# Kernel optimization log

Hardware: AMD Instinct MI355X
Metric: run time of the kernel (lower is better)

The kernel has to match this reference:

```python
import jax, jax.numpy as jnp
import numpy as np

EMB = 512
HEADS = 8

def setup_inputs() -> dict:
    key = jax.random.key(0)
    ks = jax.random.split(key, 9)
    s = 1.0 / np.sqrt(EMB)
    x = jax.random.normal(ks[0], (32, 4096, EMB), dtype=jnp.float32)
    Wq = jax.random.normal(ks[1], (EMB, EMB), dtype=jnp.float32) * s
    bq = jax.random.normal(ks[2], (EMB,), dtype=jnp.float32) * s
    Wk = jax.random.normal(ks[3], (EMB, EMB), dtype=jnp.float32) * s
    bk = jax.random.normal(ks[4], (EMB,), dtype=jnp.float32) * s
    Wv = jax.random.normal(ks[5], (EMB, EMB), dtype=jnp.float32) * s
    bv = jax.random.normal(ks[6], (EMB,), dtype=jnp.float32) * s
    Wo = jax.random.normal(ks[7], (EMB, EMB), dtype=jnp.float32) * s
    bo = jax.random.normal(ks[8], (EMB,), dtype=jnp.float32) * s
    return {"x": x, "Wq": Wq, "bq": bq, "Wk": Wk, "bk": bk,
            "Wv": Wv, "bv": bv, "Wo": Wo, "bo": bo}

def reference(x, Wq, bq, Wk, bk, Wv, bv, Wo, bo):
    b, n, e = x.shape
    h = HEADS
    d = e // h
    scale = jnp.asarray(d ** 0.5, x.dtype)
    # torch Linear: y = x @ W.T + b
    q = (x @ Wq.T + bq).reshape(b, n, h, d)
    k = (x @ Wk.T + bk).reshape(b, n, h, d)
    v = (x @ Wv.T + bv).reshape(b, n, h, d)
    # NOTE: contracts over sequence axis n (faithful to original einsum),
    # producing a (b, h, d, d) feature-feature score matrix.
    qk = jnp.einsum('bnhq,bnhk->bhqk', q, k) / scale
    attn = jax.nn.softmax(qk, axis=-1)  # softmax over head_dim axis
    # dropout is identity at inference
    weighted = jnp.einsum('bhqk,bnhk->bnhq', attn, v).reshape(b, n, e)
    return weighted @ Wo.T + bo
```

## Files before the change

kernel.cpp:

```cpp
#include <hip/hip_runtime.h>
#include <hip/hip_bf16.h>
#include <stdint.h>

#define BATCH 32
#define SEQ   4096
#define EMB   512
#define HEADS 8
#define HD    64
#define SCALE 0.125f

typedef __attribute__((ext_vector_type(8))) short bf16x8;
typedef __attribute__((ext_vector_type(4))) float f32x4;

__device__ __forceinline__ unsigned short f2bf(float f) {
    union { float f; unsigned int u; } v; v.f = f;
    unsigned int u = v.u;
    return (unsigned short)((u + 0x7FFFu + ((u >> 16) & 1u)) >> 16);
}
__device__ __forceinline__ float bf2f(unsigned short h) {
    union { unsigned int u; float f; } v; v.u = ((unsigned int)h) << 16;
    return v.f;
}
__device__ __forceinline__ unsigned int cvtpk(float lo, float hi) {
    unsigned int r;
    asm("v_cvt_pk_bf16_f32 %0, %1, %2" : "=v"(r) : "v"(lo), "v"(hi));
    return r;
}
__device__ __forceinline__ float lo_as_f(unsigned int p) {
    union { unsigned int u; float f; } v; v.u = p << 16; return v.f;
}
__device__ __forceinline__ float hi_as_f(unsigned int p) {
    union { unsigned int u; float f; } v; v.u = p & 0xFFFF0000u; return v.f;
}

#define MFMA16(a, b, c) __builtin_amdgcn_mfma_f32_16x16x32_bf16((a), (b), (c), 0, 0, 0)

union F4 { float4 v; float f[4]; };
struct Regs { F4 a0, a1, a2, a3; };

template <int NCHUNK, bool XBF>
__global__ __launch_bounds__(1024) void k1_gram(const float* __restrict__ x,
                                                float* __restrict__ P,
                                                float* __restrict__ svp,
                                                unsigned short* __restrict__ xbf) {
  constexpr int KC  = SEQ / NCHUNK;
  constexpr int NIT = KC / 32;
  constexpr int NWG = BATCH * 4 * NCHUNK;
  constexpr int PER = NWG / 8;
  const int bid = blockIdx.x;
  const int wk  = (bid & 7) * PER + (bid >> 3);
  const int c   = (NCHUNK == 2) ? (wk & 1) : 0;
  const int tt  = (NCHUNK == 2) ? ((wk >> 1) & 3) : (wk & 3);
  const int b   = (NCHUNK == 2) ? (wk >> 3) : (wk >> 2);
  const int mt = (tt >> 1) & 1, nt = tt & 1;
  const int m0 = mt * 256, n0 = nt * 256;
  const bool diag = (mt == nt);
  const float* __restrict__ xb = x + (size_t)b * SEQ * EMB;
  const int kbeg = c * KC;

  __shared__ unsigned short L[2][64 * 148];
  __shared__ float SR[256][8];

  const int tid  = threadIdx.x;
  const int lane = tid & 63;
  const int wave = tid >> 6;
  const int wr = (wave >> 2) * 64;
  const int wc = (wave & 3) * 64;
  const int er  = lane & 15;
  const int kb8 = (lane >> 4) * 8;

  const int fg   = lane;
  const int kgrp = wave >> 1;
  const bool isB = (wave & 1);
  const int pcol = isB ? n0 : m0;
  const bool active = (!diag) || (!isB);

  f32x4 acc[4][4];
#pragma unroll
  for (int i = 0; i < 4; ++i)
#pragma unroll
    for (int j = 0; j < 4; ++j) acc[i][j] = (f32x4){0.f, 0.f, 0.f, 0.f};

  float sacc[4] = {0.f, 0.f, 0.f, 0.f};

  Regs r0;

  auto loadreg = [&](int t) {
    const float* p = &xb[(size_t)(kbeg + t * 32 + kgrp * 4) * EMB + pcol + fg * 4];
    r0.a0.v = *(const float4*)p;
    r0.a1.v = *(const float4*)(p + EMB);
    r0.a2.v = *(const float4*)(p + 2 * EMB);
    r0.a3.v = *(const float4*)(p + 3 * EMB);
  };

  auto stage = [&](int t) {
    unsigned short* __restrict__ Ld = &L[isB ? 1 : 0][0];
#pragma unroll
    for (int i = 0; i < 4; ++i) {
      uint2 w;
      w.x = cvtpk(r0.a0.f[i], r0.a1.f[i]);
      w.y = cvtpk(r0.a2.f[i], r0.a3.f[i]);
      *(uint2*)&Ld[fg * 148 + i * 36 + kgrp * 4] = w;
    }
    if (diag) {
#pragma unroll
      for (int i = 0; i < 4; ++i)
        sacc[i] += (r0.a0.f[i] + r0.a1.f[i]) + (r0.a2.f[i] + r0.a3.f[i]);
      if (XBF) {
        unsigned short* xp = &xbf[((size_t)b * SEQ + kbeg + t * 32 + kgrp * 4) * EMB + m0 + fg * 4];
        uint2 xr;
        xr.x = cvtpk(r0.a0.f[0], r0.a0.f[1]); xr.y = cvtpk(r0.a0.f[2], r0.a0.f[3]);
        *(uint2*)&xp[0] = xr;
        xr.x = cvtpk(r0.a1.f[0], r0.a1.f[1]); xr.y = cvtpk(r0.a1.f[2], r0.a1.f[3]);
        *(uint2*)&xp[EMB] = xr;
        xr.x = cvtpk(r0.a2.f[0], r0.a2.f[1]); xr.y = cvtpk(r0.a2.f[2], r0.a2.f[3]);
        *(uint2*)&xp[2 * EMB] = xr;
        xr.x = cvtpk(r0.a3.f[0], r0.a3.f[1]); xr.y = cvtpk(r0.a3.f[2], r0.a3.f[3]);
        *(uint2*)&xp[3 * EMB] = xr;
      }
    }
  };

  auto frag = [&](const unsigned short* __restrict__ Ls, int e) -> bf16x8 {
    const int off = (e >> 2) * 148 + (e & 3) * 36 + kb8;
    union { bf16x8 v; uint2 u[2]; } r;
    r.u[0] = *(const uint2*)&Ls[off];
    r.u[1] = *(const uint2*)&Ls[off + 4];
    return r.v;
  };

  if (active) loadreg(0);

  for (int it = 0; it < NIT; ++it) {
    __syncthreads();
    if (active) stage(it);
    __syncthreads();
    if (active && (it + 1 < NIT)) loadreg(it + 1);

    const unsigned short* __restrict__ LAs = &L[0][0];
    const unsigned short* __restrict__ LBs = diag ? LAs : &L[1][0];
    bf16x8 bfr[4];
#pragma unroll
    for (int ns = 0; ns < 4; ++ns) bfr[ns] = frag(LBs, wc + ns * 16 + er);
    {
      bf16x8 a0f = frag(LAs, wr + er);
      bf16x8 a1f = frag(LAs, wr + 16 + er);
#pragma unroll
      for (int ns = 0; ns < 4; ++ns) {
        acc[0][ns] = MFMA16(a0f, bfr[ns], acc[0][ns]);
        acc[1][ns] = MFMA16(a1f, bfr[ns], acc[1][ns]);
      }
    }
    {
      bf16x8 a2f = frag(LAs, wr + 32 + er);
      bf16x8 a3f = frag(LAs, wr + 48 + er);
#pragma unroll
      for (int ns = 0; ns < 4; ++ns) {
        acc[2][ns] = MFMA16(a2f, bfr[ns], acc[2][ns]);
        acc[3][ns] = MFMA16(a3f, bfr[ns], acc[3][ns]);
      }
    }
  }

  float* __restrict__ Pc = P + (size_t)(c * BATCH + b) * EMB * EMB;
#pragma unroll
  for (int ms = 0; ms < 4; ++ms)
#pragma unroll
    for (int ns = 0; ns < 4; ++ns)
#pragma unroll
      for (int r = 0; r < 4; ++r) {
        const int row = m0 + wr + ms * 16 + ((lane >> 4) * 4) + r;
        const int col = n0 + wc + ns * 16 + (lane & 15);
        Pc[(size_t)row * EMB + col] = acc[ms][ns][r];
      }

  if (diag) {
    __syncthreads();
    if (!isB) {
#pragma unroll
      for (int i = 0; i < 4; ++i) SR[fg * 4 + i][kgrp] = sacc[i];
    }
    __syncthreads();
    if (tid < 256) {
      float v = 0.f;
#pragma unroll
      for (int j = 0; j < 8; ++j) v += SR[tid][j];
      svp[(size_t)(c * BATCH + b) * EMB + m0 + tid] = v;
    }
  }
}

template <bool TWO>
__global__ __launch_bounds__(256) void k2a_wqg(const float* __restrict__ Wq,
                                               const float* __restrict__ P,
                                               float* __restrict__ A) {
  const int bid = blockIdx.x;
  const int wk  = (bid & 7) * 64 + (bid >> 3);
  const int b  = wk >> 4;
  const int mt = (wk >> 2) & 3;
  const int nt = wk & 3;
  const int m0 = mt * 128, n0 = nt * 128;
  const float* __restrict__ P0b = P + (size_t)b * EMB * EMB;
  const float* __restrict__ P1b = P + (size_t)(BATCH + b) * EMB * EMB;

  __shared__ unsigned short LA[128][40];
  __shared__ unsigned short LBhi[128][40];
  __shared__ unsigned short LBlo[128][40];

  const int tid  = threadIdx.x;
  const int lane = tid & 63;
  const int wave = tid >> 6;
  const int wr = (wave >> 1) * 64;
  const int wc = (wave & 1) * 64;

  f32x4 acc[4][4];
#pragma unroll
  for (int i = 0; i < 4; ++i)
#pragma unroll
    for (int j = 0; j < 4; ++j) acc[i][j] = (f32x4){0.f, 0.f, 0.f, 0.f};

  const int rA = tid >> 3, fgA = tid & 7;

  for (int k0 = 0; k0 < EMB; k0 += 32) {
    __syncthreads();
#pragma unroll
    for (int it = 0; it < 4; ++it) {
      const int r = rA + it * 32;
      const float4 v = *(const float4*)&Wq[(size_t)(m0 + r) * EMB + k0 + fgA * 4];
      uint2 u; u.x = cvtpk(v.x, v.y); u.y = cvtpk(v.z, v.w);
      *(uint2*)&LA[r][fgA * 4] = u;
    }
#pragma unroll
    for (int it = 0; it < 4; ++it) {
      const int r = rA + it * 32;
      float4 v = *(const float4*)&P0b[(size_t)(n0 + r) * EMB + k0 + fgA * 4];
      if (TWO) {
        const float4 v1 = *(const float4*)&P1b[(size_t)(n0 + r) * EMB + k0 + fgA * 4];
        v.x += v1.x; v.y += v1.y; v.z += v1.z; v.w += v1.w;
      }
      uint2 h; h.x = cvtpk(v.x, v.y); h.y = cvtpk(v.z, v.w);
      uint2 l;
      l.x = cvtpk(v.x - lo_as_f(h.x), v.y - hi_as_f(h.x));
      l.y = cvtpk(v.z - lo_as_f(h.y), v.w - hi_as_f(h.y));
      *(uint2*)&LBhi[r][fgA * 4] = h;
      *(uint2*)&LBlo[r][fgA * 4] = l;
    }
    __syncthreads();
    bf16x8 af[4], bh[4], bl[4];
#pragma unroll
    for (int ms = 0; ms < 4; ++ms)
      af[ms] = *(const bf16x8*)&LA[wr + ms*16 + (lane & 15)][(lane >> 4) * 8];
#pragma unroll
    for (int ns = 0; ns < 4; ++ns) {
      bh[ns] = *(const bf16x8*)&LBhi[wc + ns*16 + (lane & 15)][(lane >> 4) * 8];
      bl[ns] = *(const bf16x8*)&LBlo[wc + ns*16 + (lane & 15)][(lane >> 4) * 8];
    }
#pragma unroll
    for (int ms = 0; ms < 4; ++ms)
#pragma unroll
      for (int ns = 0; ns < 4; ++ns) {
        acc[ms][ns] = MFMA16(af[ms], bh[ns], acc[ms][ns]);
        acc[ms][ns] = MFMA16(af[ms], bl[ns], acc[ms][ns]);
      }
  }

  float* __restrict__ Ab = A + (size_t)b * EMB * EMB;
#pragma unroll
  for (int ms = 0; ms < 4; ++ms)
#pragma unroll
    for (int ns = 0; ns < 4; ++ns)
#pragma unroll
      for (int r = 0; r < 4; ++r) {
        const int row = m0 + wr + ms*16 + ((lane >> 4) * 4) + r;
        const int col = n0 + wc + ns*16 + (lane & 15);
        Ab[(size_t)row * EMB + col] = acc[ms][ns][r];
      }
}

template <int NCHUNK>
__global__ __launch_bounds__(256) void k2b_logits(const float* __restrict__ A,
                                                  const float* __restrict__ Wq,
                                                  const float* __restrict__ Wk,
                                                  const float* __restrict__ bq,
                                                  const float* __restrict__ bk,
                                                  const float* __restrict__ svp,
                                                  unsigned short* __restrict__ attn) {
  const int blk = blockIdx.x;
  const int b = blk >> 3;
  const int h = blk & 7;
  const float* __restrict__ Ab = A + (size_t)b * EMB * EMB + (size_t)h * HD * EMB;

  __shared__ unsigned short LAhi[64][40];
  __shared__ unsigned short LAlo[64][40];
  __shared__ unsigned short LB[64][40];
  __shared__ float U[HD], W[HD];

  const int tid  = threadIdx.x;
  const int lane = tid & 63;
  const int wave = tid >> 6;

  if (tid < 128) {
    const int q = tid & 63;
    const float* __restrict__ wrow = (tid < 64 ? Wq : Wk) + (size_t)(h * HD + q) * EMB;
    float a = 0.f;
    for (int i = 0; i < EMB; i += 4) {
      const float4 wv = *(const float4*)&wrow[i];
      float4 sv = *(const float4*)&svp[(size_t)b * EMB + i];
      if (NCHUNK == 2) {
        const float4 s1 = *(const float4*)&svp[(size_t)(BATCH + b) * EMB + i];
        sv.x += s1.x; sv.y += s1.y; sv.z += s1.z; sv.w += s1.w;
      }
      a += wv.x*sv.x + wv.y*sv.y + wv.z*sv.z + wv.w*sv.w;
    }
    if (tid < 64) U[q] = a; else W[q] = a;
  }

  f32x4 acc[4];
#pragma unroll
  for (int i = 0; i < 4; ++i) acc[i] = (f32x4){0.f, 0.f, 0.f, 0.f};

  const int r8 = tid >> 3, fg8 = tid & 7;

  for (int k0 = 0; k0 < EMB; k0 += 32) {
    __syncthreads();
#pragma unroll
    for (int it = 0; it < 2; ++it) {
      const int r = r8 + it * 32;
      const float4 v = *(const float4*)&Ab[(size_t)r * EMB + k0 + fg8 * 4];
      uint2 h2; h2.x = cvtpk(v.x, v.y); h2.y = cvtpk(v.z, v.w);
      uint2 l2;
      l2.x = cvtpk(v.x - lo_as_f(h2.x), v.y - hi_as_f(h2.x));
      l2.y = cvtpk(v.z - lo_as_f(h2.y), v.w - hi_as_f(h2.y));
      *(ushort4*)&LAhi[r][fg8*4] = *(ushort4*)&h2;
      *(ushort4*)&LAlo[r][fg8*4] = *(ushort4*)&l2;
      const float4 wv = *(const float4*)&Wk[(size_t)(h*HD + r) * EMB + k0 + fg8 * 4];
      uint2 ub; ub.x = cvtpk(wv.x, wv.y); ub.y = cvtpk(wv.z, wv.w);
      *(ushort4*)&LB[r][fg8*4] = *(ushort4*)&ub;
    }
    __syncthreads();
    const bf16x8 ah = *(const bf16x8*)&LAhi[wave*16 + (lane & 15)][(lane >> 4) * 8];
    const bf16x8 al = *(const bf16x8*)&LAlo[wave*16 + (lane & 15)][(lane >> 4) * 8];
#pragma unroll
    for (int ns = 0; ns < 4; ++ns) {
      const bf16x8 bb = *(const bf16x8*)&LB[ns*16 + (lane & 15)][(lane >> 4) * 8];
      acc[ns] = MFMA16(ah, bb, acc[ns]);
      acc[ns] = MFMA16(al, bb, acc[ns]);
    }
  }

  const int colb = lane & 15;
  float bkv[4], wv_[4];
#pragma unroll
  for (int ns = 0; ns < 4; ++ns) {
    bkv[ns] = bk[h*HD + ns*16 + colb];
    wv_[ns] = W[ns*16 + colb];
  }
  unsigned short* __restrict__ ab = attn + (size_t)(b * HEADS + h) * HD * HD;
#pragma unroll
  for (int r = 0; r < 4; ++r) {
    const int row = wave*16 + ((lane >> 4) * 4) + r;
    const float bqv = bq[h*HD + row];
    const float uv  = U[row];
    float vals[4];
#pragma unroll
    for (int ns = 0; ns < 4; ++ns)
      vals[ns] = (acc[ns][r] + uv * bkv[ns] + bqv * wv_[ns] + 4096.f * bqv * bkv[ns]) * SCALE;
    float mx = fmaxf(fmaxf(vals[0], vals[1]), fmaxf(vals[2], vals[3]));
#pragma unroll
    for (int m = 1; m < 16; m <<= 1) mx = fmaxf(mx, __shfl_xor(mx, m));
    float sum = 0.f;
#pragma unroll
    for (int ns = 0; ns < 4; ++ns) { vals[ns] = expf(vals[ns] - mx); sum += vals[ns]; }
#pragma unroll
    for (int m = 1; m < 16; m <<= 1) sum += __shfl_xor(sum, m);
    const float inv = 1.f / sum;
#pragma unroll
    for (int ns = 0; ns < 4; ++ns)
      ab[(size_t)row * HD + ns*16 + colb] = f2bf(vals[ns] * inv);
  }
}

__global__ __launch_bounds__(256) void k3a_c(const float* __restrict__ Wo,
                                             const unsigned short* __restrict__ attn,
                                             unsigned short* __restrict__ C) {
  const int blk = blockIdx.x;
  const int b  = blk >> 5;
  const int h  = (blk >> 2) & 7;
  const int mt = blk & 3;
  const int m0 = mt * 128;

  __shared__ unsigned short LA[128][72];
  __shared__ unsigned short LB[64][72];

  const int tid  = threadIdx.x;
  const int lane = tid & 63;
  const int wave = tid >> 6;

  {
    const int r  = tid >> 4;
    const int fg = tid & 15;
#pragma unroll
    for (int it = 0; it < 8; ++it) {
      const int rr = r + it * 16;
      const float4 v = *(const float4*)&Wo[(size_t)(m0 + rr) * EMB + h*HD + fg * 4];
      uint2 u; u.x = cvtpk(v.x, v.y); u.y = cvtpk(v.z, v.w);
      *(uint2*)&LA[rr][fg * 4] = u;
    }
  }
  {
    const unsigned short* __restrict__ ab = attn + (size_t)(b * HEADS + h) * HD * HD;
#pragma unroll
    for (int it = 0; it < 16; ++it) {
      const int f  = tid + 256 * it;
      const int q  = f >> 6;
      const int kp = f & 63;
      LB[kp][q] = ab[q * HD + kp];
    }
  }
  __syncthreads();

  f32x4 acc[2][4];
#pragma unroll
  for (int i = 0; i < 2; ++i)
#pragma unroll
    for (int j = 0; j < 4; ++j) acc[i][j] = (f32x4){0.f, 0.f, 0.f, 0.f};

#pragma unroll
  for (int kk = 0; kk < 2; ++kk) {
    bf16x8 af[2], bfr[4];
#pragma unroll
    for (int ms = 0; ms < 2; ++ms)
      af[ms] = *(const bf16x8*)&LA[wave*32 + ms*16 + (lane & 15)][kk*32 + (lane >> 4) * 8];
#pragma unroll
    for (int ns = 0; ns < 4; ++ns)
      bfr[ns] = *(const bf16x8*)&LB[ns*16 + (lane & 15)][kk*32 + (lane >> 4) * 8];
#pragma unroll
    for (int ms = 0; ms < 2; ++ms)
#pragma unroll
      for (int ns = 0; ns < 4; ++ns)
        acc[ms][ns] = MFMA16(af[ms], bfr[ns], acc[ms][ns]);
  }

  unsigned short* __restrict__ Cb = C + (size_t)b * EMB * EMB;
#pragma unroll
  for (int ms = 0; ms < 2; ++ms)
#pragma unroll
    for (int ns = 0; ns < 4; ++ns)
#pragma unroll
      for (int r = 0; r < 4; ++r) {
        const int row = m0 + wave*32 + ms*16 + ((lane >> 4) * 4) + r;
        const int col = h*HD + ns*16 + (lane & 15);
        Cb[(size_t)row * EMB + col] = f2bf(acc[ms][ns][r]);
      }
}

__global__ __launch_bounds__(256) void k3b_d(const unsigned short* __restrict__ C,
                                             const float* __restrict__ Wv,
                                             unsigned short* __restrict__ D) {
  const int bid = blockIdx.x;
  const int wk  = (bid & 7) * 64 + (bid >> 3);
  const int b  = wk >> 4;
  const int mt = (wk >> 2) & 3;
  const int nt = wk & 3;
  const int m0 = mt * 128, n0 = nt * 128;
  const unsigned short* __restrict__ Cb = C + (size_t)b * EMB * EMB;

  __shared__ unsigned short LA[128][40];
  __shared__ unsigned short LB[128][40];

  const int tid  = threadIdx.x;
  const int lane = tid & 63;
  const int wave = tid >> 6;
  const int wr = (wave >> 1) * 64;
  const int wc = (wave & 1) * 64;

  f32x4 acc[4][4];
#pragma unroll
  for (int i = 0; i < 4; ++i)
#pragma unroll
    for (int j = 0; j < 4; ++j) acc[i][j] = (f32x4){0.f, 0.f, 0.f, 0.f};

  const int kl = tid >> 5, fgB = tid & 31;
  const int rA = tid >> 3, fgA = tid & 7;

  for (int k0 = 0; k0 < EMB; k0 += 32) {
    __syncthreads();
#pragma unroll
    for (int it = 0; it < 4; ++it) {
      const int r = rA + it * 32;
      *(ushort4*)&LA[r][fgA*4] = *(const ushort4*)&Cb[(size_t)(m0 + r) * EMB + k0 + fgA * 4];
    }
#pragma unroll
    for (int it = 0; it < 4; ++it) {
      const int k = kl + it * 8;
      const float4 v = *(const float4*)&Wv[(size_t)(k0 + k) * EMB + n0 + fgB * 4];
      LB[fgB*4+0][k] = f2bf(v.x);
      LB[fgB*4+1][k] = f2bf(v.y);
      LB[fgB*4+2][k] = f2bf(v.z);
      LB[fgB*4+3][k] = f2bf(v.w);
    }
    __syncthreads();
    bf16x8 af[4], bfr[4];
#pragma unroll
    for (int ms = 0; ms < 4; ++ms)
      af[ms] = *(const bf16x8*)&LA[wr + ms*16 + (lane & 15)][(lane >> 4) * 8];
#pragma unroll
    for (int ns = 0; ns < 4; ++ns)
      bfr[ns] = *(const bf16x8*)&LB[wc + ns*16 + (lane & 15)][(lane >> 4) * 8];
#pragma unroll
    for (int ms = 0; ms < 4; ++ms)
#pragma unroll
      for (int ns = 0; ns < 4; ++ns)
        acc[ms][ns] = MFMA16(af[ms], bfr[ns], acc[ms][ns]);
  }

  unsigned short* __restrict__ Db = D + (size_t)b * EMB * EMB;
#pragma unroll
  for (int ms = 0; ms < 4; ++ms)
#pragma unroll
    for (int ns = 0; ns < 4; ++ns)
#pragma unroll
      for (int r = 0; r < 4; ++r) {
        const int row = m0 + wr + ms*16 + ((lane >> 4) * 4) + r;
        const int col = n0 + wc + ns*16 + (lane & 15);
        Db[(size_t)row * EMB + col] = f2bf(acc[ms][ns][r]);
      }
}

__global__ __launch_bounds__(256) void k3c_e(const unsigned short* __restrict__ C,
                                             const float* __restrict__ bv,
                                             const float* __restrict__ bo,
                                             float* __restrict__ evec) {
  const int blk = blockIdx.x;
  const int b = blk >> 4;
  const int g = blk & 15;
  const int tid  = threadIdx.x;
  const int lane = tid & 63;
  const int wave = tid >> 6;

  __shared__ float BV[EMB];
  for (int i = tid; i < EMB; i += 256) BV[i] = bv[i];
  __syncthreads();

  const unsigned short* __restrict__ Cb = C + (size_t)b * EMB * EMB;
#pragma unroll
  for (int p = 0; p < 8; ++p) {
    const int row = g*32 + wave*8 + p;
    const unsigned short* cr = &Cb[(size_t)row * EMB + lane * 8];
    const float* bvp = &BV[lane * 8];
    ushort4 v0 = *(const ushort4*)&cr[0];
    ushort4 v1 = *(const ushort4*)&cr[4];
    float a = bf2f(v0.x)*bvp[0] + bf2f(v0.y)*bvp[1] + bf2f(v0.z)*bvp[2] + bf2f(v0.w)*bvp[3]
            + bf2f(v1.x)*bvp[4] + bf2f(v1.y)*bvp[5] + bf2f(v1.z)*bvp[6] + bf2f(v1.w)*bvp[7];
#pragma unroll
    for (int m = 1; m < 64; m <<= 1) a += __shfl_xor(a, m);
    if (lane == 0) evec[b * EMB + row] = a + bo[row];
  }
}

template <bool XBF>
__global__ __launch_bounds__(1024) void k4_out(const float* __restrict__ x,
                                               const unsigned short* __restrict__ xbf,
                                               const unsigned short* __restrict__ D,
                                               const float* __restrict__ evec,
                                               float* __restrict__ out) {
  const int bid = blockIdx.x;
  const int wk  = (bid & 7) * 128 + (bid >> 3);
  const int b  = wk >> 5;
  const int mt = (wk >> 1) & 15;
  const int nt = wk & 1;
  const int m0 = mt * 256, n0 = nt * 256;
  const float* __restrict__ xb = x + (size_t)b * SEQ * EMB;
  const unsigned short* __restrict__ xbb = xbf + (size_t)b * SEQ * EMB;
  const unsigned short* __restrict__ Db = D + (size_t)b * EMB * EMB;

  __shared__ unsigned short L[2][256 * 40];

  const int tid  = threadIdx.x;
  const int lane = tid & 63;
  const int wave = tid >> 6;
  const int wr = (wave >> 2) * 64;
  const int wc = (wave & 3) * 64;
  const int er  = lane & 15;
  const int kb8 = (lane >> 4) * 8;

  const int rs = tid >> 2;
  const int kg = tid & 3;

  f32x4 acc[4][4];
#pragma unroll
  for (int i = 0; i < 4; ++i)
#pragma unroll
    for (int j = 0; j < 4; ++j) acc[i][j] = (f32x4){0.f, 0.f, 0.f, 0.f};

  uint4 ua, ub;
  F4 fa0, fa1;

  auto loadreg = [&](int k0) {
    if (XBF) {
      ua = *(const uint4*)&xbb[(size_t)(m0 + rs) * EMB + k0 + kg * 8];
    } else {
      fa0.v = *(const float4*)&xb[(size_t)(m0 + rs) * EMB + k0 + kg * 8];
      fa1.v = *(const float4*)&xb[(size_t)(m0 + rs) * EMB + k0 + kg * 8 + 4];
    }
    ub = *(const uint4*)&Db[(size_t)(n0 + rs) * EMB + k0 + kg * 8];
  };

  auto stage = [&]() {
    if (XBF) {
      *(uint4*)&L[0][rs * 40 + kg * 8] = ua;
    } else {
      uint4 w;
      w.x = cvtpk(fa0.f[0], fa0.f[1]); w.y = cvtpk(fa0.f[2], fa0.f[3]);
      w.z = cvtpk(fa1.f[0], fa1.f[1]); w.w = cvtpk(fa1.f[2], fa1.f[3]);
      *(uint4*)&L[0][rs * 40 + kg * 8] = w;
    }
    *(uint4*)&L[1][rs * 40 + kg * 8] = ub;
  };

  auto frag = [&](const unsigned short* __restrict__ Ls, int e) -> bf16x8 {
    return *(const bf16x8*)&Ls[e * 40 + kb8];
  };

  loadreg(0);

  for (int it = 0; it < 16; ++it) {
    __syncthreads();
    stage();
    __syncthreads();
    if (it + 1 < 16) loadreg((it + 1) * 32);

    const unsigned short* __restrict__ LAs = &L[0][0];
    const unsigned short* __restrict__ LBs = &L[1][0];
    bf16x8 bfr[4];
#pragma unroll
    for (int ns = 0; ns < 4; ++ns) bfr[ns] = frag(LBs, wc + ns * 16 + er);
    {
      bf16x8 a0f = frag(LAs, wr + er);
      bf16x8 a1f = frag(LAs, wr + 16 + er);
#pragma unroll
      for (int ns = 0; ns < 4; ++ns) {
        acc[0][ns] = MFMA16(a0f, bfr[ns], acc[0][ns]);
        acc[1][ns] = MFMA16(a1f, bfr[ns], acc[1][ns]);
      }
    }
    {
      bf16x8 a2f = frag(LAs, wr + 32 + er);
      bf16x8 a3f = frag(LAs, wr + 48 + er);
#pragma unroll
      for (int ns = 0; ns < 4; ++ns) {
        acc[2][ns] = MFMA16(a2f, bfr[ns], acc[2][ns]);
        acc[3][ns] = MFMA16(a3f, bfr[ns], acc[3][ns]);
      }
    }
  }

  float ev4[4];
#pragma unroll
  for (int ns = 0; ns < 4; ++ns)
    ev4[ns] = evec[b * EMB + n0 + wc + ns * 16 + (lane & 15)];

#pragma unroll
  for (int ms = 0; ms < 4; ++ms)
#pragma unroll
    for (int ns = 0; ns < 4; ++ns)
#pragma unroll
      for (int r = 0; r < 4; ++r) {
        const int row = m0 + wr + ms * 16 + ((lane >> 4) * 4) + r;
        const int col = n0 + wc + ns * 16 + (lane & 15);
        out[((size_t)b * SEQ + row) * EMB + col] = acc[ms][ns][r] + ev4[ns];
      }
}

extern "C" void kernel_launch(void* const* d_in, const int* in_sizes, int n_in,
                              void* d_out, int out_size, void* d_ws, size_t ws_size,
                              hipStream_t stream) {
  (void)in_sizes; (void)n_in; (void)out_size;
  const float* x  = (const float*)d_in[0];
  const float* Wq = (const float*)d_in[1];
  const float* bq = (const float*)d_in[2];
  const float* Wk = (const float*)d_in[3];
  const float* bk = (const float*)d_in[4];
  const float* Wv = (const float*)d_in[5];
  const float* bv = (const float*)d_in[6];
  const float* Wo = (const float*)d_in[7];
  const float* bo = (const float*)d_in[8];
  float* out = (float*)d_out;

  char* ws = (char*)d_ws;
  const size_t MB = (size_t)1 << 20;
  const size_t XBF_BYTES = (size_t)BATCH * SEQ * EMB * 2;
  const size_t NEED2 = XBF_BYTES + 98 * MB + 256 * 1024;
  const size_t NEED1 = XBF_BYTES + 66 * MB + 256 * 1024;

  if (ws_size >= NEED2) {
    unsigned short* xbf  = (unsigned short*)(ws);
    float*          P    = (float*)(ws + XBF_BYTES);
    unsigned short* Cm   = (unsigned short*)(ws + XBF_BYTES);
    unsigned short* Dm   = (unsigned short*)(ws + XBF_BYTES + 16 * MB);
    float*          A    = (float*)(ws + XBF_BYTES + 64 * MB);
    unsigned short* attn = (unsigned short*)(ws + XBF_BYTES + 96 * MB);
    float*          svp  = (float*)(ws + XBF_BYTES + 98 * MB);
    float*          ev   = (float*)(ws + XBF_BYTES + 98 * MB + 192 * 1024);

    hipLaunchKernelGGL((k1_gram<2, true>), dim3(BATCH * 8),  dim3(1024), 0, stream, x, P, svp, xbf);
    hipLaunchKernelGGL((k2a_wqg<true>),    dim3(BATCH * 16), dim3(256), 0, stream, Wq, P, A);
    hipLaunchKernelGGL((k2b_logits<2>),    dim3(BATCH * 8),  dim3(256), 0, stream, A, Wq, Wk, bq, bk, svp, attn);
    hipLaunchKernelGGL(k3a_c,              dim3(BATCH * 32), dim3(256), 0, stream, Wo, attn, Cm);
    hipLaunchKernelGGL(k3b_d,              dim3(BATCH * 16), dim3(256), 0, stream, Cm, Wv, Dm);
    hipLaunchKernelGGL(k3c_e,              dim3(BATCH * 16), dim3(256), 0, stream, Cm, bv, bo, ev);
    hipLaunchKernelGGL((k4_out<true>),     dim3(BATCH * 32), dim3(1024), 0, stream, x, xbf, Dm, ev, out);
  } else if (ws_size >= NEED1) {
    unsigned short* xbf  = (unsigned short*)(ws);
    float*          P    = (float*)(ws + XBF_BYTES);
    unsigned short* Cm   = (unsigned short*)(ws + XBF_BYTES);
    unsigned short* Dm   = (unsigned short*)(ws + XBF_BYTES + 16 * MB);
    float*          A    = (float*)(ws + XBF_BYTES + 32 * MB);
    unsigned short* attn = (unsigned short*)(ws + XBF_BYTES + 64 * MB);
    float*          svp  = (float*)(ws + XBF_BYTES + 66 * MB);
    float*          ev   = (float*)(ws + XBF_BYTES + 66 * MB + 192 * 1024);

    hipLaunchKernelGGL((k1_gram<1, true>), dim3(BATCH * 4),  dim3(1024), 0, stream, x, P, svp, xbf);
    hipLaunchKernelGGL((k2a_wqg<false>),   dim3(BATCH * 16), dim3(256), 0, stream, Wq, P, A);
    hipLaunchKernelGGL((k2b_logits<1>),    dim3(BATCH * 8),  dim3(256), 0, stream, A, Wq, Wk, bq, bk, svp, attn);
    hipLaunchKernelGGL(k3a_c,              dim3(BATCH * 32), dim3(256), 0, stream, Wo, attn, Cm);
    hipLaunchKernelGGL(k3b_d,              dim3(BATCH * 16), dim3(256), 0, stream, Cm, Wv, Dm);
    hipLaunchKernelGGL(k3c_e,              dim3(BATCH * 16), dim3(256), 0, stream, Cm, bv, bo, ev);
    hipLaunchKernelGGL((k4_out<true>),     dim3(BATCH * 32), dim3(1024), 0, stream, x, xbf, Dm, ev, out);
  } else {
    unsigned short* xbf  = (unsigned short*)(ws);
    float*          P    = (float*)(ws);
    unsigned short* Cm   = (unsigned short*)(ws);
    unsigned short* Dm   = (unsigned short*)(ws + 16 * MB);
    float*          A    = (float*)(ws + 32 * MB);
    unsigned short* attn = (unsigned short*)(ws + 64 * MB);
    float*          svp  = (float*)(ws + 66 * MB);
    float*          ev   = (float*)(ws + 66 * MB + 192 * 1024);

    hipLaunchKernelGGL((k1_gram<1, false>), dim3(BATCH * 4),  dim3(1024), 0, stream, x, P, svp, xbf);
    hipLaunchKernelGGL((k2a_wqg<false>),    dim3(BATCH * 16), dim3(256), 0, stream, Wq, P, A);
    hipLaunchKernelGGL((k2b_logits<1>),     dim3(BATCH * 8),  dim3(256), 0, stream, A, Wq, Wk, bq, bk, svp, attn);
    hipLaunchKernelGGL(k3a_c,               dim3(BATCH * 32), dim3(256), 0, stream, Wo, attn, Cm);
    hipLaunchKernelGGL(k3b_d,               dim3(BATCH * 16), dim3(256), 0, stream, Cm, Wv, Dm);
    hipLaunchKernelGGL(k3c_e,               dim3(BATCH * 16), dim3(256), 0, stream, Cm, bv, bo, ev);
    hipLaunchKernelGGL((k4_out<false>),     dim3(BATCH * 32), dim3(1024), 0, stream, x, xbf, Dm, ev, out);
  }
}
```

Baseline: 374.5 us.

## Retile output GEMM to full-width rows and repack Wv staging layout

The final output GEMM now gives each 1024-thread block a 128-row by 512-column tile instead of 256x256. Each x row is therefore read and converted once rather than twice, but the full 512-row D slice is staged in shared memory on every k-step. The k3b_d kernel also changes how the Wv tile is transposed into shared memory: it uses packed 2-element conversions and uint2 stores into a padded layout instead of scalar 16-bit scatter stores, which reduces LDS store count and bank conflicts. The larger B tile raises LDS use and D traffic per block, and fragment loads for Wv become two 8-byte reads.

```diff
diff --git a/kernel.cpp b/kernel.cpp
--- a/kernel.cpp
+++ b/kernel.cpp
@@ -466,13 +466,15 @@
   const unsigned short* __restrict__ Cb = C + (size_t)b * EMB * EMB;
 
   __shared__ unsigned short LA[128][40];
-  __shared__ unsigned short LB[128][40];
+  __shared__ unsigned short LB[32 * 148];
 
   const int tid  = threadIdx.x;
   const int lane = tid & 63;
   const int wave = tid >> 6;
   const int wr = (wave >> 1) * 64;
   const int wc = (wave & 1) * 64;
+  const int er  = lane & 15;
+  const int kb8 = (lane >> 4) * 8;
 
   f32x4 acc[4][4];
 #pragma unroll
@@ -480,8 +482,9 @@
 #pragma unroll
     for (int j = 0; j < 4; ++j) acc[i][j] = (f32x4){0.f, 0.f, 0.f, 0.f};
 
-  const int kl = tid >> 5, fgB = tid & 31;
   const int rA = tid >> 3, fgA = tid & 7;
+  const int fgB = tid & 31;
+  const int kgB = tid >> 5;
 
   for (int k0 = 0; k0 < EMB; k0 += 32) {
     __syncthreads();
@@ -490,23 +493,35 @@
       const int r = rA + it * 32;
       *(ushort4*)&LA[r][fgA*4] = *(const ushort4*)&Cb[(size_t)(m0 + r) * EMB + k0 + fgA * 4];
     }
-#pragma unroll
-    for (int it = 0; it < 4; ++it) {
-      const int k = kl + it * 8;
-      const float4 v = *(const float4*)&Wv[(size_t)(k0 + k) * EMB + n0 + fgB * 4];
-      LB[fgB*4+0][k] = f2bf(v.x);
-      LB[fgB*4+1][k] = f2bf(v.y);
-      LB[fgB*4+2][k] = f2bf(v.z);
-      LB[fgB*4+3][k] = f2bf(v.w);
+    {
+      const float* p = &Wv[(size_t)(k0 + kgB * 4) * EMB + n0 + fgB * 4];
+      F4 b0, b1, b2, b3;
+      b0.v = *(const float4*)p;
+      b1.v = *(const float4*)(p + EMB);
+      b2.v = *(const float4*)(p + 2 * EMB);
+      b3.v = *(const float4*)(p + 3 * EMB);
+#pragma unroll
+      for (int i = 0; i < 4; ++i) {
+        uint2 w;
+        w.x = cvtpk(b0.f[i], b1.f[i]);
+        w.y = cvtpk(b2.f[i], b3.f[i]);
+        *(uint2*)&LB[fgB * 148 + i * 36 + kgB * 4] = w;
+      }
     }
     __syncthreads();
     bf16x8 af[4], bfr[4];
 #pragma unroll
     for (int ms = 0; ms < 4; ++ms)
-      af[ms] = *(const bf16x8*)&LA[wr + ms*16 + (lane & 15)][(lane >> 4) * 8];
-#pragma unroll
-    for (int ns = 0; ns < 4; ++ns)
-      bfr[ns] = *(const bf16x8*)&LB[wc + ns*16 + (lane & 15)][(lane >> 4) * 8];
+      af[ms] = *(const bf16x8*)&LA[wr + ms*16 + er][kb8];
+#pragma unroll
+    for (int ns = 0; ns < 4; ++ns) {
+      const int e = wc + ns * 16 + er;
+      const int off = (e >> 2) * 148 + (e & 3) * 36 + kb8;
+      union { bf16x8 v; uint2 u[2]; } r;
+      r.u[0] = *(const uint2*)&LB[off];
+      r.u[1] = *(const uint2*)&LB[off + 4];
+      bfr[ns] = r.v;
+    }
 #pragma unroll
     for (int ms = 0; ms < 4; ++ms)
 #pragma unroll
@@ -567,25 +582,27 @@
   const int bid = blockIdx.x;
   const int wk  = (bid & 7) * 128 + (bid >> 3);
   const int b  = wk >> 5;
-  const int mt = (wk >> 1) & 15;
-  const int nt = wk & 1;
-  const int m0 = mt * 256, n0 = nt * 256;
+  const int mt = wk & 31;
+  const int m0 = mt * 128;
   const float* __restrict__ xb = x + (size_t)b * SEQ * EMB;
   const unsigned short* __restrict__ xbb = xbf + (size_t)b * SEQ * EMB;
   const unsigned short* __restrict__ Db = D + (size_t)b * EMB * EMB;
 
-  __shared__ unsigned short L[2][256 * 40];
+  __shared__ unsigned short LA[128 * 40];
+  __shared__ unsigned short LB[512 * 40];
 
   const int tid  = threadIdx.x;
   const int lane = tid & 63;
   const int wave = tid >> 6;
-  const int wr = (wave >> 2) * 64;
-  const int wc = (wave & 3) * 64;
+  const int wr = (wave >> 3) * 64;
+  const int wc = (wave & 7) * 64;
   const int er  = lane & 15;
   const int kb8 = (lane >> 4) * 8;
 
-  const int rs = tid >> 2;
-  const int kg = tid & 3;
+  const int rsA = tid >> 3;
+  const int kgA = tid & 7;
+  const int rsB = tid >> 1;
+  const int kgB = (tid & 1) * 16;
 
   f32x4 acc[4][4];
 #pragma unroll
@@ -593,35 +610,31 @@
 #pragma unroll
     for (int j = 0; j < 4; ++j) acc[i][j] = (f32x4){0.f, 0.f, 0.f, 0.f};
 
-  uint4 ua, ub;
-  F4 fa0, fa1;
+  uint2 ua;
+  F4 fa;
+  uint4 ub0, ub1;
 
   auto loadreg = [&](int k0) {
     if (XBF) {
-      ua = *(const uint4*)&xbb[(size_t)(m0 + rs) * EMB + k0 + kg * 8];
+      ua = *(const uint2*)&xbb[(size_t)(m0 + rsA) * EMB + k0 + kgA * 4];
     } else {
-      fa0.v = *(const float4*)&xb[(size_t)(m0 + rs) * EMB + k0 + kg * 8];
-      fa1.v = *(const float4*)&xb[(size_t)(m0 + rs) * EMB + k0 + kg * 8 + 4];
-    }
-    ub = *(const uint4*)&Db[(size_t)(n0 + rs) * EMB + k0 + kg * 8];
+      fa.v = *(const float4*)&xb[(size_t)(m0 + rsA) * EMB + k0 + kgA * 4];
+    }
+    ub0 = *(const uint4*)&Db[(size_t)rsB * EMB + k0 + kgB];
+    ub1 = *(const uint4*)&Db[(size_t)rsB * EMB + k0 + kgB + 8];
   };
 
   auto stage = [&]() {
     if (XBF) {
-      *(uint4*)&L[0][rs * 40 + kg * 8] = ua;
+      *(uint2*)&LA[rsA * 40 + kgA * 4] = ua;
     } else {
-      uint4 w;
-      w.x = cvtpk(fa0.f[0], fa0.f[1]); w.y = cvtpk(fa0.f[2], fa0.f[3]);
-      w.z = cvtpk(fa1.f[0], fa1.f[1]); w.w = cvtpk(fa1.f[2], fa1.f[3]);
-      *(uint4*)&L[0][rs * 40 + kg * 8] = w;
-    }
-    *(uint4*)&L[1][rs * 40 + kg * 8] = ub;
+      uint2 w; w.x = cvtpk(fa.f[0], fa.f[1]); w.y = cvtpk(fa.f[2], fa.f[3]);
+      *(uint2*)&LA[rsA * 40 + kgA * 4] = w;
+    }
+    *(uint4*)&LB[rsB * 40 + kgB] = ub0;
+    *(uint4*)&LB[rsB * 40 + kgB + 8] = ub1;
   };
 
-  auto frag = [&](const unsigned short* __restrict__ Ls, int e) -> bf16x8 {
-    return *(const bf16x8*)&Ls[e * 40 + kb8];
-  };
-
   loadreg(0);
 
   for (int it = 0; it < 16; ++it) {
@@ -630,14 +643,13 @@
     __syncthreads();
     if (it + 1 < 16) loadreg((it + 1) * 32);
 
-    const unsigned short* __restrict__ LAs = &L[0][0];
-    const unsigned short* __restrict__ LBs = &L[1][0];
     bf16x8 bfr[4];
 #pragma unroll
-    for (int ns = 0; ns < 4; ++ns) bfr[ns] = frag(LBs, wc + ns * 16 + er);
+    for (int ns = 0; ns < 4; ++ns)
+      bfr[ns] = *(const bf16x8*)&LB[(wc + ns * 16 + er) * 40 + kb8];
     {
-      bf16x8 a0f = frag(LAs, wr + er);
-      bf16x8 a1f = frag(LAs, wr + 16 + er);
+      bf16x8 a0f = *(const bf16x8*)&LA[(wr + er) * 40 + kb8];
+      bf16x8 a1f = *(const bf16x8*)&LA[(wr + 16 + er) * 40 + kb8];
 #pragma unroll
       for (int ns = 0; ns < 4; ++ns) {
         acc[0][ns] = MFMA16(a0f, bfr[ns], acc[0][ns]);
@@ -645,8 +657,8 @@
       }
     }
     {
-      bf16x8 a2f = frag(LAs, wr + 32 + er);
-      bf16x8 a3f = frag(LAs, wr + 48 + er);
+      bf16x8 a2f = *(const bf16x8*)&LA[(wr + 32 + er) * 40 + kb8];
+      bf16x8 a3f = *(const bf16x8*)&LA[(wr + 48 + er) * 40 + kb8];
 #pragma unroll
       for (int ns = 0; ns < 4; ++ns) {
         acc[2][ns] = MFMA16(a2f, bfr[ns], acc[2][ns]);
@@ -658,7 +670,7 @@
   float ev4[4];
 #pragma unroll
   for (int ns = 0; ns < 4; ++ns)
-    ev4[ns] = evec[b * EMB + n0 + wc + ns * 16 + (lane & 15)];
+    ev4[ns] = evec[b * EMB + wc + ns * 16 + (lane & 15)];
 
 #pragma unroll
   for (int ms = 0; ms < 4; ++ms)
@@ -667,7 +679,7 @@
 #pragma unroll
       for (int r = 0; r < 4; ++r) {
         const int row = m0 + wr + ms * 16 + ((lane >> 4) * 4) + r;
-        const int col = n0 + wc + ns * 16 + (lane & 15);
+        const int col = wc + ns * 16 + (lane & 15);
         out[((size_t)b * SEQ + row) * EMB + col] = acc[ms][ns][r] + ev4[ns];
       }
 }
```

Result: faster. 363.2 us (-3.0%).
